# Kernel tuning notes

Hardware: AMD Instinct MI355X
Metric: run time of the kernel (lower is better)

Reference implementation:

```python
import jax, jax.numpy as jnp
import numpy as np

B, N, C = 2, 2048, 1024
H = 16
D = C // H
HID = 4 * C
EPS = 1e-5


def layernorm(x, g, b):
    mu = jnp.mean(x, axis=-1, keepdims=True)
    var = jnp.var(x, axis=-1, keepdims=True)
    return (x - mu) * jax.lax.rsqrt(var + EPS) * g + b


def setup_inputs() -> dict:
    key = jax.random.key(0)
    ks = jax.random.split(key, 8)
    s = lambda fan_in: 1.0 / np.sqrt(fan_in)
    return {
        "x": jax.random.normal(ks[0], (B, N, C), dtype=jnp.float32),
        "ln1_g": jnp.ones((C,), jnp.float32),
        "ln1_b": jnp.zeros((C,), jnp.float32),
        "w_qkv": jax.random.normal(ks[1], (C, 3 * C), jnp.float32) * s(C),
        "w_proj": jax.random.normal(ks[2], (C, C), jnp.float32) * s(C),
        "b_proj": jnp.zeros((C,), jnp.float32),
        "ln2_g": jnp.ones((C,), jnp.float32),
        "ln2_b": jnp.zeros((C,), jnp.float32),
        "w_fc1": jax.random.normal(ks[3], (C, HID), jnp.float32) * s(C),
        "b_fc1": jnp.zeros((HID,), jnp.float32),
        "w_fc2": jax.random.normal(ks[4], (HID, C), jnp.float32) * s(HID),
        "b_fc2": jnp.zeros((C,), jnp.float32),
        "metadata": 0,
        "thw_shape": 2048,
    }


def reference(x, ln1_g, ln1_b, w_qkv, w_proj, b_proj, ln2_g, ln2_b,
              w_fc1, b_fc1, w_fc2, b_fc2, metadata, thw_shape):
    scale = 1.0 / np.sqrt(D)
    # --- attention branch (pre-norm) ---
    xn = layernorm(x, ln1_g, ln1_b)
    qkv = (xn @ w_qkv).reshape(B, N, 3, H, D)
    q = jnp.transpose(qkv[:, :, 0], (0, 2, 1, 3))  # [B,H,N,D]
    k = jnp.transpose(qkv[:, :, 1], (0, 2, 1, 3))
    v = jnp.transpose(qkv[:, :, 2], (0, 2, 1, 3))
    attn = jax.nn.softmax(jnp.einsum('bhnd,bhmd->bhnm', q, k) * scale, axis=-1)
    o = jnp.einsum('bhnm,bhmd->bhnd', attn, v)
    o = jnp.transpose(o, (0, 2, 1, 3)).reshape(B, N, C)
    x = x + (o @ w_proj + b_proj)
    # --- MLP branch (pre-norm) ---
    xn2 = layernorm(x, ln2_g, ln2_b)
    h = jax.nn.gelu(xn2 @ w_fc1 + b_fc1, approximate=False)  # torch GELU = exact erf
    x = x + (h @ w_fc2 + b_fc2)
    return x
```

## Files before the change

### kernel.cpp

```cpp
#include <hip/hip_runtime.h>

#define B_   2
#define N_   2048
#define C_   1024
#define H_   16
#define D_   64
#define HID_ 4096
#define M_   (B_ * N_)

typedef __attribute__((ext_vector_type(8))) short bf16x8;
typedef __attribute__((ext_vector_type(4))) float f32x4;

__device__ __forceinline__ unsigned short f2bf(float f) {
  unsigned int u = __builtin_bit_cast(unsigned int, f);
  u += 0x7fffu + ((u >> 16) & 1u);
  return (unsigned short)(u >> 16);
}

__device__ __forceinline__ unsigned int cvtpk(float a, float b) {
  unsigned int r;
  asm("v_cvt_pk_bf16_f32 %0, %1, %2" : "=v"(r) : "v"(a), "v"(b));
  return r;
}

__device__ __forceinline__ float exp2a(float x) {
  float r;
  asm("v_exp_f32 %0, %1" : "=v"(r) : "v"(x));
  return r;
}

__device__ __forceinline__ void gl2lds16(const void* g, void* l) {
  __builtin_amdgcn_global_load_lds(
      (const __attribute__((address_space(1))) unsigned int*)g,
      (__attribute__((address_space(3))) unsigned int*)l, 16, 0, 0);
}

#define LOG2E 1.44269504088896f

__global__ __launch_bounds__(256) void ln_kernel(const float* __restrict__ x,
                                                 const float* __restrict__ g,
                                                 const float* __restrict__ bta,
                                                 unsigned short* __restrict__ out) {
  int row  = blockIdx.x * 4 + (threadIdx.x >> 6);
  int lane = threadIdx.x & 63;
  const float* xr = x + (size_t)row * C_;
  float4 v[4];
  float s1 = 0.f, s2 = 0.f;
#pragma unroll
  for (int j = 0; j < 4; j++) {
    v[j] = *(const float4*)(xr + j * 256 + lane * 4);
    s1 += v[j].x + v[j].y + v[j].z + v[j].w;
    s2 += v[j].x * v[j].x + v[j].y * v[j].y + v[j].z * v[j].z + v[j].w * v[j].w;
  }
#pragma unroll
  for (int m = 1; m < 64; m <<= 1) { s1 += __shfl_xor(s1, m); s2 += __shfl_xor(s2, m); }
  float mu  = s1 * (1.0f / C_);
  float var = s2 * (1.0f / C_) - mu * mu;
  float rs  = rsqrtf(var + 1e-5f);
#pragma unroll
  for (int j = 0; j < 4; j++) {
    const float4 gv = *(const float4*)(g + j * 256 + lane * 4);
    const float4 bv = *(const float4*)(bta + j * 256 + lane * 4);
    ushort4 o;
    o.x = f2bf((v[j].x - mu) * rs * gv.x + bv.x);
    o.y = f2bf((v[j].y - mu) * rs * gv.y + bv.y);
    o.z = f2bf((v[j].z - mu) * rs * gv.z + bv.z);
    o.w = f2bf((v[j].w - mu) * rs * gv.w + bv.w);
    *(ushort4*)(out + (size_t)row * C_ + j * 256 + lane * 4) = o;
  }
}

__global__ __launch_bounds__(256) void prep_kernel(
    const float* __restrict__ x, const float* __restrict__ ln1g,
    const float* __restrict__ ln1b, unsigned short* __restrict__ xn,
    const float* __restrict__ w0, const float* __restrict__ w1,
    const float* __restrict__ w2, const float* __restrict__ w3,
    unsigned short* __restrict__ o0, unsigned short* __restrict__ o1,
    unsigned short* __restrict__ o2, unsigned short* __restrict__ o3) {
  __shared__ float t[32][33];
  int bid = blockIdx.x, tid = threadIdx.x;
  if (bid < 1024) {
    int row  = bid * 4 + (tid >> 6);
    int lane = tid & 63;
    const float* xr = x + (size_t)row * C_;
    float4 v[4];
    float s1 = 0.f, s2 = 0.f;
#pragma unroll
    for (int j = 0; j < 4; j++) {
      v[j] = *(const float4*)(xr + j * 256 + lane * 4);
      s1 += v[j].x + v[j].y + v[j].z + v[j].w;
      s2 += v[j].x * v[j].x + v[j].y * v[j].y + v[j].z * v[j].z + v[j].w * v[j].w;
    }
#pragma unroll
    for (int m = 1; m < 64; m <<= 1) { s1 += __shfl_xor(s1, m); s2 += __shfl_xor(s2, m); }
    float mu  = s1 * (1.0f / C_);
    float var = s2 * (1.0f / C_) - mu * mu;
    float rs  = rsqrtf(var + 1e-5f);
#pragma unroll
    for (int j = 0; j < 4; j++) {
      const float4 gv = *(const float4*)(ln1g + j * 256 + lane * 4);
      const float4 bv = *(const float4*)(ln1b + j * 256 + lane * 4);
      ushort4 o;
      o.x = f2bf((v[j].x - mu) * rs * gv.x + bv.x);
      o.y = f2bf((v[j].y - mu) * rs * gv.y + bv.y);
      o.z = f2bf((v[j].z - mu) * rs * gv.z + bv.z);
      o.w = f2bf((v[j].w - mu) * rs * gv.w + bv.w);
      *(ushort4*)(xn + (size_t)row * C_ + j * 256 + lane * 4) = o;
    }
    return;
  }
  int id = bid - 1024;
  const float* W; unsigned short* Wt; int K, N, rel;
  if (id < 3072)      { W = w0; Wt = o0; K = 1024; N = 3072; rel = id; }
  else if (id < 4096) { W = w1; Wt = o1; K = 1024; N = 1024; rel = id - 3072; }
  else if (id < 8192) { W = w2; Wt = o2; K = 1024; N = 4096; rel = id - 4096; }
  else                { W = w3; Wt = o3; K = 4096; N = 1024; rel = id - 8192; }
  int nx = N >> 5;
  int n0 = (rel % nx) * 32, k0 = (rel / nx) * 32;
  int tx = tid & 31, ty = tid >> 5;
#pragma unroll
  for (int j = 0; j < 4; j++)
    t[ty + j * 8][tx] = W[(size_t)(k0 + ty + j * 8) * N + n0 + tx];
  __syncthreads();
#pragma unroll
  for (int j = 0; j < 4; j++)
    Wt[(size_t)(n0 + ty + j * 8) * K + k0 + tx] = f2bf(t[tx][ty + j * 8]);
}

__global__ __launch_bounds__(256) void gemm_db_kernel(
    const unsigned short* __restrict__ A,
    const unsigned short* __restrict__ Wt,
    const float* __restrict__ bias,
    const float* __restrict__ resid,
    float* __restrict__ outf,
    int M, int N, int K) {
  __shared__ __align__(16) short As[2][128][64];
  __shared__ __align__(16) short Bs[2][64][64];
  int tid = threadIdx.x;
  int w = tid >> 6, lane = tid & 63, r = lane & 15, quad = lane >> 4;
  int rowbase = w * 32;

  int nwg = gridDim.x * gridDim.y;
  int lin = blockIdx.y * gridDim.x + blockIdx.x;
  int cpx = nwg >> 3;
  lin = (lin & 7) * cpx + (lin >> 3);
  int bx = lin % gridDim.x, by = lin / gridDim.x;
  int bM = by * 128, bN = bx * 64;

  int srow   = (w << 3) + (lane >> 3);
  int schunk = (lane & 7) ^ ((lane >> 3) & 7);
  const unsigned short* aP = A  + (size_t)(bM + srow) * K + schunk * 8;
  const unsigned short* bP = Wt + (size_t)(bN + srow) * K + schunk * 8;

  int pc0 = (quad ^ (r & 7)) * 8;

  f32x4 acc[2][4];
#pragma unroll
  for (int i = 0; i < 2; i++)
#pragma unroll
    for (int j = 0; j < 4; j++) acc[i][j] = f32x4{0.f, 0.f, 0.f, 0.f};

#define STAGE_DB(kt, b)                                                       \
  do {                                                                        \
    int k0_ = (kt) * 64;                                                      \
    _Pragma("unroll") for (int p = 0; p < 4; p++)                             \
      gl2lds16(aP + (size_t)(p * 32) * K + k0_, &As[b][p * 32 + (w << 3)][0]);\
    _Pragma("unroll") for (int p = 0; p < 2; p++)                             \
      gl2lds16(bP + (size_t)(p * 32) * K + k0_, &Bs[b][p * 32 + (w << 3)][0]);\
  } while (0)

  const int nk = K >> 6;
  STAGE_DB(0, 0);
  __syncthreads();

  for (int kt = 0; kt < nk; kt++) {
    const int cb = kt & 1;
    if (kt + 1 < nk) STAGE_DB(kt + 1, cb ^ 1);
#pragma unroll
    for (int kh = 0; kh < 2; kh++) {
      int pc = pc0 ^ (kh * 32);
      bf16x8 af[2], bfr[4];
#pragma unroll
      for (int mt = 0; mt < 2; mt++)
        af[mt] = *(const bf16x8*)&As[cb][rowbase + mt * 16 + r][pc];
#pragma unroll
      for (int nt = 0; nt < 4; nt++)
        bfr[nt] = *(const bf16x8*)&Bs[cb][nt * 16 + r][pc];
#pragma unroll
      for (int mt = 0; mt < 2; mt++)
#pragma unroll
        for (int nt = 0; nt < 4; nt++)
          acc[mt][nt] = __builtin_amdgcn_mfma_f32_16x16x32_bf16(af[mt], bfr[nt], acc[mt][nt], 0, 0, 0);
    }
    __syncthreads();
  }

#pragma unroll
  for (int mt = 0; mt < 2; mt++) {
#pragma unroll
    for (int nt = 0; nt < 4; nt++) {
#pragma unroll
      for (int i = 0; i < 4; i++) {
        int gm = bM + rowbase + mt * 16 + quad * 4 + i;
        int gn = bN + nt * 16 + r;
        outf[(size_t)gm * N + gn] = acc[mt][nt][i] + bias[gn] + resid[(size_t)gm * N + gn];
      }
    }
  }
#undef STAGE_DB
}

template <int MODE>
__global__ __launch_bounds__(512, 2) void gemm256_kernel(
    const unsigned short* __restrict__ A,
    const unsigned short* __restrict__ Wt,
    const float* __restrict__ bias,
    unsigned short* __restrict__ outb0,
    unsigned short* __restrict__ outb1,
    unsigned short* __restrict__ outb2,
    int M, int N, int K) {
  __shared__ __align__(16) short As[2][256][64];
  __shared__ __align__(16) short Bs[2][256][64];
  const int tid = threadIdx.x;
  const int w = tid >> 6, lane = tid & 63, r = lane & 15, quad = lane >> 4;
  const int wr = w >> 2, wc = w & 3;
  const int bN = blockIdx.x * 256, bM = blockIdx.y * 256;

  const int srow   = (w << 3) + (lane >> 3);
  const int schunk = (lane & 7) ^ ((lane >> 3) & 7);
  const unsigned short* aSrc = A  + (size_t)(bM + srow) * K + schunk * 8;
  const unsigned short* bSrc = Wt + (size_t)(bN + srow) * K + schunk * 8;
  const int wrow = w << 3;

  const int ntiles = K >> 6;
  const int tmask  = ntiles - 1;

#define STAGE_H(t, h)                                                            \
  do {                                                                           \
    int b_ = (t) & 1, tt_ = (t) & tmask;                                         \
    if ((h) < 2) {                                                               \
      const unsigned short* p_ = aSrc + (size_t)((h) * 128) * K + tt_ * 64;      \
      gl2lds16(p_, &As[b_][(h) * 128 + wrow][0]);                                \
      gl2lds16(p_ + (size_t)64 * K, &As[b_][(h) * 128 + 64 + wrow][0]);          \
    } else {                                                                     \
      const unsigned short* p_ = bSrc + (size_t)(((h) - 2) * 128) * K + tt_ * 64;\
      gl2lds16(p_, &Bs[b_][((h) - 2) * 128 + wrow][0]);                          \
      gl2lds16(p_ + (size_t)64 * K, &Bs[b_][((h) - 2) * 128 + 64 + wrow][0]);    \
    }                                                                            \
  } while (0)

  f32x4 acc[8][4];
#pragma unroll
  for (int i = 0; i < 8; i++)
#pragma unroll
    for (int j = 0; j < 4; j++) acc[i][j] = f32x4{0.f, 0.f, 0.f, 0.f};

  bf16x8 af[4][2];
  bf16x8 bfr[4][2];

#define RD_A(b, msub)                                                            \
  {                                                                              \
    _Pragma("unroll") for (int mt_ = 0; mt_ < 4; mt_++)                          \
      _Pragma("unroll") for (int ks_ = 0; ks_ < 2; ks_++)                        \
        af[mt_][ks_] = *(const bf16x8*)&As[b][wr * 128 + (msub) * 64 + mt_ * 16 + r] \
                                          [((ks_ * 4 + quad) ^ (r & 7)) * 8];    \
  }
#define RD_B(b, nh)                                                              \
  {                                                                              \
    _Pragma("unroll") for (int nt_ = 0; nt_ < 2; nt_++)                          \
      _Pragma("unroll") for (int ks_ = 0; ks_ < 2; ks_++)                        \
        bfr[(nh) * 2 + nt_][ks_] =                                               \
            *(const bf16x8*)&Bs[b][wc * 64 + (nh) * 32 + nt_ * 16 + r]           \
                               [((ks_ * 4 + quad) ^ (r & 7)) * 8];               \
  }
#define MM_Q(msub, nh)                                                           \
  {                                                                              \
    _Pragma("unroll") for (int mt_ = 0; mt_ < 4; mt_++)                          \
      _Pragma("unroll") for (int nt_ = 0; nt_ < 2; nt_++)                        \
        _Pragma("unroll") for (int ks_ = 0; ks_ < 2; ks_++)                      \
          acc[(msub) * 4 + mt_][(nh) * 2 + nt_] =                                \
              __builtin_amdgcn_mfma_f32_16x16x32_bf16(                           \
                  af[mt_][ks_], bfr[(nh) * 2 + nt_][ks_],                        \
                  acc[(msub) * 4 + mt_][(nh) * 2 + nt_], 0, 0, 0);               \
  }

#define BARRIER() asm volatile("s_barrier" ::: "memory")
#define WAITL()   asm volatile("s_waitcnt lgkmcnt(0)" ::: "memory")
#define WAITV2()  asm volatile("s_waitcnt vmcnt(2)" ::: "memory")
#define PRIO1()   __builtin_amdgcn_s_setprio(1)
#define PRIO0()   __builtin_amdgcn_s_setprio(0)

  STAGE_H(0, 0); STAGE_H(0, 1); STAGE_H(0, 2); STAGE_H(0, 3);
  STAGE_H(1, 0);
  WAITV2();
  BARRIER();

  const int niter = ntiles >> 1;
  for (int i = 0; i < niter; i++) {
    const int tc = 2 * i;
    RD_A(0, 0); RD_B(0, 0);
    STAGE_H(tc + 1, 1);
    BARRIER(); WAITL();
    PRIO1(); MM_Q(0, 0); PRIO0();
    BARRIER();
    RD_B(0, 1);
    STAGE_H(tc + 1, 2);
    BARRIER(); WAITL();
    PRIO1(); MM_Q(0, 1); PRIO0();
    BARRIER();
    RD_A(0, 1);
    STAGE_H(tc + 1, 3);
    BARRIER(); WAITL();
    PRIO1(); MM_Q(1, 1); PRIO0();
    BARRIER();
    STAGE_H(tc + 2, 0);
    BARRIER(); WAITL();
    PRIO1(); MM_Q(1, 0); PRIO0();
    WAITV2();
    BARRIER();
    RD_A(1, 0); RD_B(1, 0);
    STAGE_H(tc + 2, 1);
    BARRIER(); WAITL();
    PRIO1(); MM_Q(0, 0); PRIO0();
    BARRIER();
    RD_B(1, 1);
    STAGE_H(tc + 2, 2);
    BARRIER(); WAITL();
    PRIO1(); MM_Q(0, 1); PRIO0();
    BARRIER();
    RD_A(1, 1);
    STAGE_H(tc + 2, 3);
    BARRIER(); WAITL();
    PRIO1(); MM_Q(1, 1); PRIO0();
    BARRIER();
    STAGE_H(tc + 3, 0);
    BARRIER(); WAITL();
    PRIO1(); MM_Q(1, 0); PRIO0();
    WAITV2();
    BARRIER();
  }

#pragma unroll
  for (int m = 0; m < 8; m++) {
#pragma unroll
    for (int n = 0; n < 4; n++) {
      int gm0 = bM + wr * 128 + m * 16 + quad * 4;
      int gn  = bN + wc * 64 + n * 16 + r;
      if (MODE == 0) {
        int s = gn >> 10, c = gn & 1023;
        int hh = c >> 6, d = c & 63;
        int b = gm0 >> 11, n0 = gm0 & 2047;
        if (s == 2) {
          unsigned int p0 = cvtpk(acc[m][n][0], acc[m][n][1]);
          unsigned int p1 = cvtpk(acc[m][n][2], acc[m][n][3]);
          *(uint2*)(outb2 + ((size_t)(b * H_ + hh) * D_ + d) * N_ + n0) = uint2{p0, p1};
        } else {
          unsigned short* dst = (s == 0) ? outb0 : outb1;
          float sc = (s == 0) ? 0.125f * LOG2E : 1.0f;
#pragma unroll
          for (int i2 = 0; i2 < 4; i2++) {
            size_t di = ((size_t)(b * H_ + hh) * N_ + n0 + i2) * D_ + d;
            dst[di] = f2bf(acc[m][n][i2] * sc);
          }
        }
      } else {
#pragma unroll
        for (int i2 = 0; i2 < 4; i2++) {
          float t = acc[m][n][i2] + bias[gn];
          float gl = 0.5f * t * (1.0f + erff(t * 0.70710678118f));
          outb0[(size_t)(gm0 + i2) * N + gn] = f2bf(gl);
        }
      }
    }
  }
#undef STAGE_H
#undef RD_A
#undef RD_B
#undef MM_Q
#undef BARRIER
#undef WAITL
#undef WAITV2
#undef PRIO1
#undef PRIO0
}

__global__ __launch_bounds__(512, 2) void attn_kernel(const unsigned short* __restrict__ qb,
                                                      const unsigned short* __restrict__ kb,
                                                      const unsigned short* __restrict__ vtb,
                                                      unsigned short* __restrict__ ob) {
  __shared__ __align__(16) short Ks[2][128][64];
  __shared__ __align__(16) short Vts[2][64][128];
  __shared__ __align__(16) short Pl[8 * 16 * 128];
  int tid = threadIdx.x;
  int w = tid >> 6, lane = tid & 63, r = lane & 15, quad = lane >> 4;
  int bh = blockIdx.x & 31, qt = blockIdx.x >> 5;
  const unsigned short* qh  = qb  + (size_t)bh * N_ * D_;
  const unsigned short* kh  = kb  + (size_t)bh * N_ * D_;
  const unsigned short* vth = vtb + (size_t)bh * D_ * N_;
  int swz = r & 7;

  bf16x8 qf[2][2];
#pragma unroll
  for (int mt = 0; mt < 2; mt++)
#pragma unroll
    for (int ks = 0; ks < 2; ks++)
      qf[mt][ks] = *(const bf16x8*)(qh + (size_t)(qt * 256 + w * 32 + mt * 16 + r) * D_ + ks * 32 + quad * 8);

  float mst[2] = {-1e30f, -1e30f}, lst[2] = {0.f, 0.f};
  f32x4 oacc[2][4];
#pragma unroll
  for (int mt = 0; mt < 2; mt++)
#pragma unroll
    for (int nt = 0; nt < 4; nt++) oacc[mt][nt] = f32x4{0.f, 0.f, 0.f, 0.f};

  const unsigned short* kBase = kh + (size_t)(tid >> 3) * D_ + ((tid & 7) ^ ((tid >> 3) & 7)) * 8;
  const unsigned short* vBase = vth + (size_t)(tid >> 4) * N_ + ((tid & 15) ^ ((tid >> 4) & 7)) * 8;

  short* Plw = &Pl[0] + w * 2048;

  gl2lds16(kBase,                        &Ks[0][(w << 3)][0]);
  gl2lds16(kBase + (size_t)64 * D_,      &Ks[0][64 + (w << 3)][0]);
  gl2lds16(vBase,                        &Vts[0][(w << 2)][0]);
  gl2lds16(vBase + (size_t)32 * N_,      &Vts[0][32 + (w << 2)][0]);
  __syncthreads();

  for (int t = 0; t < 16; t++) {
    const int cur = t & 1;
    if (t < 15) {
      const int nb = cur ^ 1;
      gl2lds16(kBase + (size_t)(t + 1) * 128 * D_,                  &Ks[nb][(w << 3)][0]);
      gl2lds16(kBase + (size_t)((t + 1) * 128 + 64) * D_,           &Ks[nb][64 + (w << 3)][0]);
      gl2lds16(vBase + (size_t)(t + 1) * 128,                       &Vts[nb][(w << 2)][0]);
      gl2lds16(vBase + (size_t)(t + 1) * 128 + (size_t)32 * N_,     &Vts[nb][32 + (w << 2)][0]);
    }

    f32x4 sacc[2][8];
#pragma unroll
    for (int mt = 0; mt < 2; mt++)
#pragma unroll
      for (int nt = 0; nt < 8; nt++) sacc[mt][nt] = f32x4{0.f, 0.f, 0.f, 0.f};
#pragma unroll
    for (int ks = 0; ks < 2; ks++) {
#pragma unroll
      for (int nt = 0; nt < 8; nt++) {
        bf16x8 kfr = *(const bf16x8*)&Ks[cur][nt * 16 + r][((ks * 4 + quad) ^ swz) * 8];
#pragma unroll
        for (int mt = 0; mt < 2; mt++)
          sacc[mt][nt] = __builtin_amdgcn_mfma_f32_16x16x32_bf16(kfr, qf[mt][ks], sacc[mt][nt], 0, 0, 0);
      }
    }

    bf16x8 vfr[4][4];
#pragma unroll
    for (int ks = 0; ks < 4; ks++)
#pragma unroll
      for (int nt2 = 0; nt2 < 4; nt2++)
        vfr[ks][nt2] = *(const bf16x8*)&Vts[cur][nt2 * 16 + r][((ks * 4 + quad) ^ swz) * 8];

#pragma unroll
    for (int mt = 0; mt < 2; mt++) {
      float tm = -1e30f;
#pragma unroll
      for (int nt = 0; nt < 8; nt++)
#pragma unroll
        for (int i = 0; i < 4; i++) tm = fmaxf(tm, sacc[mt][nt][i]);
      tm = fmaxf(tm, __shfl_xor(tm, 16));
      tm = fmaxf(tm, __shfl_xor(tm, 32));
      if (__ballot(tm > mst[mt] + 8.0f)) {
        float mnew = fmaxf(mst[mt], tm);
        float alpha = exp2a(mst[mt] - mnew);
        mst[mt] = mnew;
        lst[mt] *= alpha;
#pragma unroll
        for (int i = 0; i < 4; i++) {
          float av = __shfl(alpha, (lane & 48) | (quad * 4 + i));
#pragma unroll
          for (int nt2 = 0; nt2 < 4; nt2++) oacc[mt][nt2][i] *= av;
        }
      }
      float m = mst[mt];
      float rs = 0.f;
#pragma unroll
      for (int nt = 0; nt < 8; nt++)
#pragma unroll
        for (int i = 0; i < 4; i++) {
          float p = exp2a(sacc[mt][nt][i] - m);
          sacc[mt][nt][i] = p;
          rs += p;
        }
      rs += __shfl_xor(rs, 16);
      rs += __shfl_xor(rs, 32);
      lst[mt] += rs;
    }

#pragma unroll
    for (int mt = 0; mt < 2; mt++) {
#pragma unroll
      for (int nt = 0; nt < 8; nt++) {
        uint2 pw;
        pw.x = cvtpk(sacc[mt][nt][0], sacc[mt][nt][1]);
        pw.y = cvtpk(sacc[mt][nt][2], sacc[mt][nt][3]);
        *(uint2*)&Plw[r * 128 + (((nt * 2 + (quad >> 1)) ^ swz) * 8) + (quad & 1) * 4] = pw;
      }
      asm volatile("" ::: "memory");
#pragma unroll
      for (int ks = 0; ks < 4; ks++) {
        bf16x8 pfr = *(const bf16x8*)&Plw[r * 128 + ((ks * 4 + quad) ^ swz) * 8];
#pragma unroll
        for (int nt2 = 0; nt2 < 4; nt2++)
          oacc[mt][nt2] = __builtin_amdgcn_mfma_f32_16x16x32_bf16(pfr, vfr[ks][nt2], oacc[mt][nt2], 0, 0, 0);
      }
      asm volatile("" ::: "memory");
    }

    __syncthreads();
  }

  int bb = bh >> 4, hh = bh & 15;
#pragma unroll
  for (int mt = 0; mt < 2; mt++) {
#pragma unroll
    for (int i = 0; i < 4; i++) {
      float li = __shfl(lst[mt], (lane & 48) | (quad * 4 + i));
      float inv = 1.0f / li;
      int row = qt * 256 + w * 32 + mt * 16 + quad * 4 + i;
#pragma unroll
      for (int nt2 = 0; nt2 < 4; nt2++) {
        int d = nt2 * 16 + r;
        ob[((size_t)bb * N_ + row) * C_ + hh * D_ + d] = f2bf(oacc[mt][nt2][i] * inv);
      }
    }
  }
}

extern "C" void kernel_launch(void* const* d_in, const int* in_sizes, int n_in,
                              void* d_out, int out_size, void* d_ws, size_t ws_size,
                              hipStream_t stream) {
  const float* x     = (const float*)d_in[0];
  const float* ln1g  = (const float*)d_in[1];
  const float* ln1b  = (const float*)d_in[2];
  const float* wqkv  = (const float*)d_in[3];
  const float* wproj = (const float*)d_in[4];
  const float* bproj = (const float*)d_in[5];
  const float* ln2g  = (const float*)d_in[6];
  const float* ln2b  = (const float*)d_in[7];
  const float* wfc1  = (const float*)d_in[8];
  const float* bfc1  = (const float*)d_in[9];
  const float* wfc2  = (const float*)d_in[10];
  const float* bfc2  = (const float*)d_in[11];
  float* out = (float*)d_out;

  const size_t MB = 1u << 20;
  if (ws_size < 88 * MB) return;
  char* w = (char*)d_ws;
  unsigned short* xn    = (unsigned short*)(w + 0 * MB);
  unsigned short* qbuf  = (unsigned short*)(w + 8 * MB);
  unsigned short* kbuf  = (unsigned short*)(w + 16 * MB);
  unsigned short* hbuf  = (unsigned short*)(w + 0 * MB);
  unsigned short* obuf  = (unsigned short*)(w + 32 * MB);
  float*          x2    = (float*)         (w + 40 * MB);
  unsigned short* xn2   = (unsigned short*)(w + 56 * MB);
  unsigned short* vtb   = (unsigned short*)(w + 56 * MB);
  unsigned short* wqkvt = (unsigned short*)(w + 64 * MB);
  unsigned short* wprjt = (unsigned short*)(w + 70 * MB);
  unsigned short* wfc1t = (unsigned short*)(w + 72 * MB);
  unsigned short* wfc2t = (unsigned short*)(w + 80 * MB);

  prep_kernel<<<1024 + 12288, 256, 0, stream>>>(x, ln1g, ln1b, xn,
                                                wqkv, wproj, wfc1, wfc2,
                                                wqkvt, wprjt, wfc1t, wfc2t);

  gemm256_kernel<0><<<dim3(3 * C_ / 256, M_ / 256), 512, 0, stream>>>(
      xn, wqkvt, nullptr, qbuf, kbuf, vtb, M_, 3 * C_, C_);
  attn_kernel<<<B_ * H_ * (N_ / 256), 512, 0, stream>>>(qbuf, kbuf, vtb, obuf);
  gemm_db_kernel<<<dim3(C_ / 64, M_ / 128), 256, 0, stream>>>(
      obuf, wprjt, bproj, x, x2, M_, C_, C_);
  ln_kernel<<<M_ / 4, 256, 0, stream>>>(x2, ln2g, ln2b, xn2);
  gemm256_kernel<2><<<dim3(HID_ / 256, M_ / 256), 512, 0, stream>>>(
      xn2, wfc1t, bfc1, hbuf, nullptr, nullptr, M_, HID_, C_);
  gemm_db_kernel<<<dim3(C_ / 64, M_ / 128), 256, 0, stream>>>(
      hbuf, wfc2t, bfc2, x2, out, M_, C_, HID_);
}
```

Measured before the change: 345.3 us.

## Halve attention query tile per block and reuse K LDS buffer for P

The attention kernel now processes 128 queries per block (16 per wave) instead of 256, which doubles the grid and halves the per-wave accumulator and score registers. The separate P staging buffer in LDS is removed; P is written into the current K buffer after an added barrier, and V fragments are loaded from LDS inside the PV loop. Launch bounds are raised to allow 4 blocks per CU. The aim is higher occupancy and more blocks to hide latency. The cost is that each K/V tile is now loaded by twice as many blocks, plus one extra barrier per iteration.

```diff
diff --git a/kernel.cpp b/kernel.cpp
--- a/kernel.cpp
+++ b/kernel.cpp
@@ -384,13 +384,12 @@
 #undef PRIO0
 }
 
-__global__ __launch_bounds__(512, 2) void attn_kernel(const unsigned short* __restrict__ qb,
+__global__ __launch_bounds__(512, 4) void attn_kernel(const unsigned short* __restrict__ qb,
                                                       const unsigned short* __restrict__ kb,
                                                       const unsigned short* __restrict__ vtb,
                                                       unsigned short* __restrict__ ob) {
   __shared__ __align__(16) short Ks[2][128][64];
   __shared__ __align__(16) short Vts[2][64][128];
-  __shared__ __align__(16) short Pl[8 * 16 * 128];
   int tid = threadIdx.x;
   int w = tid >> 6, lane = tid & 63, r = lane & 15, quad = lane >> 4;
   int bh = blockIdx.x & 31, qt = blockIdx.x >> 5;
@@ -399,24 +398,18 @@
   const unsigned short* vth = vtb + (size_t)bh * D_ * N_;
   int swz = r & 7;
 
-  bf16x8 qf[2][2];
-#pragma unroll
-  for (int mt = 0; mt < 2; mt++)
-#pragma unroll
-    for (int ks = 0; ks < 2; ks++)
-      qf[mt][ks] = *(const bf16x8*)(qh + (size_t)(qt * 256 + w * 32 + mt * 16 + r) * D_ + ks * 32 + quad * 8);
-
-  float mst[2] = {-1e30f, -1e30f}, lst[2] = {0.f, 0.f};
-  f32x4 oacc[2][4];
-#pragma unroll
-  for (int mt = 0; mt < 2; mt++)
-#pragma unroll
-    for (int nt = 0; nt < 4; nt++) oacc[mt][nt] = f32x4{0.f, 0.f, 0.f, 0.f};
+  bf16x8 qf[2];
+#pragma unroll
+  for (int ks = 0; ks < 2; ks++)
+    qf[ks] = *(const bf16x8*)(qh + (size_t)(qt * 128 + w * 16 + r) * D_ + ks * 32 + quad * 8);
+
+  float mst = -1e30f, lst = 0.f;
+  f32x4 oacc[4];
+#pragma unroll
+  for (int nt = 0; nt < 4; nt++) oacc[nt] = f32x4{0.f, 0.f, 0.f, 0.f};
 
   const unsigned short* kBase = kh + (size_t)(tid >> 3) * D_ + ((tid & 7) ^ ((tid >> 3) & 7)) * 8;
   const unsigned short* vBase = vth + (size_t)(tid >> 4) * N_ + ((tid & 15) ^ ((tid >> 4) & 7)) * 8;
-
-  short* Plw = &Pl[0] + w * 2048;
 
   gl2lds16(kBase,                        &Ks[0][(w << 3)][0]);
   gl2lds16(kBase + (size_t)64 * D_,      &Ks[0][64 + (w << 3)][0]);
@@ -434,81 +427,76 @@
       gl2lds16(vBase + (size_t)(t + 1) * 128 + (size_t)32 * N_,     &Vts[nb][32 + (w << 2)][0]);
     }
 
-    f32x4 sacc[2][8];
-#pragma unroll
-    for (int mt = 0; mt < 2; mt++)
-#pragma unroll
-      for (int nt = 0; nt < 8; nt++) sacc[mt][nt] = f32x4{0.f, 0.f, 0.f, 0.f};
+    f32x4 sacc[8];
+#pragma unroll
+    for (int nt = 0; nt < 8; nt++) sacc[nt] = f32x4{0.f, 0.f, 0.f, 0.f};
 #pragma unroll
     for (int ks = 0; ks < 2; ks++) {
 #pragma unroll
       for (int nt = 0; nt < 8; nt++) {
         bf16x8 kfr = *(const bf16x8*)&Ks[cur][nt * 16 + r][((ks * 4 + quad) ^ swz) * 8];
-#pragma unroll
-        for (int mt = 0; mt < 2; mt++)
-          sacc[mt][nt] = __builtin_amdgcn_mfma_f32_16x16x32_bf16(kfr, qf[mt][ks], sacc[mt][nt], 0, 0, 0);
+        sacc[nt] = __builtin_amdgcn_mfma_f32_16x16x32_bf16(kfr, qf[ks], sacc[nt], 0, 0, 0);
       }
     }
 
-    bf16x8 vfr[4][4];
-#pragma unroll
-    for (int ks = 0; ks < 4; ks++)
-#pragma unroll
-      for (int nt2 = 0; nt2 < 4; nt2++)
-        vfr[ks][nt2] = *(const bf16x8*)&Vts[cur][nt2 * 16 + r][((ks * 4 + quad) ^ swz) * 8];
-
-#pragma unroll
-    for (int mt = 0; mt < 2; mt++) {
+    {
       float tm = -1e30f;
 #pragma unroll
       for (int nt = 0; nt < 8; nt++)
 #pragma unroll
-        for (int i = 0; i < 4; i++) tm = fmaxf(tm, sacc[mt][nt][i]);
+        for (int i = 0; i < 4; i++) tm = fmaxf(tm, sacc[nt][i]);
       tm = fmaxf(tm, __shfl_xor(tm, 16));
       tm = fmaxf(tm, __shfl_xor(tm, 32));
-      if (__ballot(tm > mst[mt] + 8.0f)) {
-        float mnew = fmaxf(mst[mt], tm);
-        float alpha = exp2a(mst[mt] - mnew);
-        mst[mt] = mnew;
-        lst[mt] *= alpha;
+      if (__ballot(tm > mst + 8.0f)) {
+        float mnew = fmaxf(mst, tm);
+        float alpha = exp2a(mst - mnew);
+        mst = mnew;
+        lst *= alpha;
 #pragma unroll
         for (int i = 0; i < 4; i++) {
           float av = __shfl(alpha, (lane & 48) | (quad * 4 + i));
 #pragma unroll
-          for (int nt2 = 0; nt2 < 4; nt2++) oacc[mt][nt2][i] *= av;
+          for (int nt2 = 0; nt2 < 4; nt2++) oacc[nt2][i] *= av;
         }
       }
-      float m = mst[mt];
+      float m = mst;
       float rs = 0.f;
 #pragma unroll
       for (int nt = 0; nt < 8; nt++)
 #pragma unroll
         for (int i = 0; i < 4; i++) {
-          float p = exp2a(sacc[mt][nt][i] - m);
-          sacc[mt][nt][i] = p;
+          float p = exp2a(sacc[nt][i] - m);
+          sacc[nt][i] = p;
           rs += p;
         }
       rs += __shfl_xor(rs, 16);
       rs += __shfl_xor(rs, 32);
-      lst[mt] += rs;
-    }
-
-#pragma unroll
-    for (int mt = 0; mt < 2; mt++) {
-#pragma unroll
-      for (int nt = 0; nt < 8; nt++) {
+      lst += rs;
+    }
+
+    __syncthreads();
+    short* Plw = &Ks[cur][0][0] + w * 1024;
+
+#pragma unroll
+    for (int khalf = 0; khalf < 2; khalf++) {
+#pragma unroll
+      for (int ntw = 0; ntw < 4; ntw++) {
+        int nt = khalf * 4 + ntw;
         uint2 pw;
-        pw.x = cvtpk(sacc[mt][nt][0], sacc[mt][nt][1]);
-        pw.y = cvtpk(sacc[mt][nt][2], sacc[mt][nt][3]);
-        *(uint2*)&Plw[r * 128 + (((nt * 2 + (quad >> 1)) ^ swz) * 8) + (quad & 1) * 4] = pw;
+        pw.x = cvtpk(sacc[nt][0], sacc[nt][1]);
+        pw.y = cvtpk(sacc[nt][2], sacc[nt][3]);
+        *(uint2*)&Plw[r * 64 + (((ntw * 2 + (quad >> 1)) ^ swz) * 8) + (quad & 1) * 4] = pw;
       }
       asm volatile("" ::: "memory");
 #pragma unroll
-      for (int ks = 0; ks < 4; ks++) {
-        bf16x8 pfr = *(const bf16x8*)&Plw[r * 128 + ((ks * 4 + quad) ^ swz) * 8];
-#pragma unroll
-        for (int nt2 = 0; nt2 < 4; nt2++)
-          oacc[mt][nt2] = __builtin_amdgcn_mfma_f32_16x16x32_bf16(pfr, vfr[ks][nt2], oacc[mt][nt2], 0, 0, 0);
+      for (int ksp = 0; ksp < 2; ksp++) {
+        int ks = khalf * 2 + ksp;
+        bf16x8 pfr = *(const bf16x8*)&Plw[r * 64 + ((ksp * 4 + quad) ^ swz) * 8];
+#pragma unroll
+        for (int nt2 = 0; nt2 < 4; nt2++) {
+          bf16x8 vfr = *(const bf16x8*)&Vts[cur][nt2 * 16 + r][((ks * 4 + quad) ^ swz) * 8];
+          oacc[nt2] = __builtin_amdgcn_mfma_f32_16x16x32_bf16(pfr, vfr, oacc[nt2], 0, 0, 0);
+        }
       }
       asm volatile("" ::: "memory");
     }
@@ -518,17 +506,14 @@
 
   int bb = bh >> 4, hh = bh & 15;
 #pragma unroll
-  for (int mt = 0; mt < 2; mt++) {
-#pragma unroll
-    for (int i = 0; i < 4; i++) {
-      float li = __shfl(lst[mt], (lane & 48) | (quad * 4 + i));
-      float inv = 1.0f / li;
-      int row = qt * 256 + w * 32 + mt * 16 + quad * 4 + i;
-#pragma unroll
-      for (int nt2 = 0; nt2 < 4; nt2++) {
-        int d = nt2 * 16 + r;
-        ob[((size_t)bb * N_ + row) * C_ + hh * D_ + d] = f2bf(oacc[mt][nt2][i] * inv);
-      }
+  for (int i = 0; i < 4; i++) {
+    float li = __shfl(lst, (lane & 48) | (quad * 4 + i));
+    float inv = 1.0f / li;
+    int row = qt * 128 + w * 16 + quad * 4 + i;
+#pragma unroll
+    for (int nt2 = 0; nt2 < 4; nt2++) {
+      int d = nt2 * 16 + r;
+      ob[((size_t)bb * N_ + row) * C_ + hh * D_ + d] = f2bf(oacc[nt2][i] * inv);
     }
   }
 }
@@ -572,7 +557,7 @@
 
   gemm256_kernel<0><<<dim3(3 * C_ / 256, M_ / 256), 512, 0, stream>>>(
       xn, wqkvt, nullptr, qbuf, kbuf, vtb, M_, 3 * C_, C_);
-  attn_kernel<<<B_ * H_ * (N_ / 256), 512, 0, stream>>>(qbuf, kbuf, vtb, obuf);
+  attn_kernel<<<B_ * H_ * (N_ / 128), 512, 0, stream>>>(qbuf, kbuf, vtb, obuf);
   gemm_db_kernel<<<dim3(C_ / 64, M_ / 128), 256, 0, stream>>>(
       obuf, wprjt, bproj, x, x2, M_, C_, C_);
   ln_kernel<<<M_ / 4, 256, 0, stream>>>(x2, ln2g, ln2b, xn2);
```

New measurement: 351.5 us. Within noise of the previous version (+1.8%).
